# Optimization experiments

Measured on AMD Instinct MI355X. Metric: run time of the kernel, lower is better.

The kernel has to match this reference:

```python
import jax, jax.numpy as jnp
import numpy as np

THETA = 0.5  # forward default arg
ALPHA = 0.2  # LeakyReLU negative slope
NEG_INF = -9e15


def setup_inputs() -> dict:
    key = jax.random.key(0)
    k1, k2, k3, k4, k5 = jax.random.split(key, 5)
    N, F_IN, F_OUT = 8192, 256, 256
    h = jax.random.normal(k1, (N, F_IN), dtype=jnp.float32)
    adj = jax.random.randint(k2, (N, N), 0, 2, dtype=jnp.int32)
    cv_values = jax.random.uniform(k3, (N,), dtype=jnp.float32)
    # xavier_uniform with gain=1.414
    g = 1.414
    bw = g * np.sqrt(6.0 / (F_IN + F_OUT))
    W = jax.random.uniform(k4, (F_IN, F_OUT), dtype=jnp.float32, minval=-bw, maxval=bw)
    ba = g * np.sqrt(6.0 / (2 * F_OUT + 1))
    a = jax.random.uniform(k5, (2 * F_OUT, 1), dtype=jnp.float32, minval=-ba, maxval=ba)
    return {"h": h, "adj": adj, "cv_values": cv_values, "W": W, "a": a}


def reference(h, adj, cv_values, W, a):
    # Wh: [N, F_out]
    Wh = h @ W
    F_out = Wh.shape[1]
    a1 = a[:F_out, 0]   # [F_out]
    a2 = a[F_out:, 0]   # [F_out]
    # e_ij = LeakyReLU([Wh_i ; Wh_j] . a) = LeakyReLU(Wh_i.a1 + Wh_j.a2)
    f1 = Wh @ a1        # [N]
    f2 = Wh @ a2        # [N]
    e = jax.nn.leaky_relu(f1[:, None] + f2[None, :], negative_slope=ALPHA)
    # CV bias: theta * cv_i broadcast across row i
    e = e + THETA * cv_values[:, None]
    att = jnp.where(adj > 0, e, jnp.float32(NEG_INF))
    att = jax.nn.softmax(att, axis=1)
    # dropout is identity in eval mode (training=False)
    h_prime = att @ Wh  # [N, F_out]
    return jax.nn.elu(h_prime)  # concat=True branch
```

## Files before the change

### kernel.cpp

```cpp
#include <hip/hip_runtime.h>
#include <cstdint>
#include <cstddef>

typedef _Float16 half8 __attribute__((ext_vector_type(8)));
typedef _Float16 half4 __attribute__((ext_vector_type(4)));
typedef float f32x4 __attribute__((ext_vector_type(4)));

#define GAT_N 8192
#define GAT_F 256
#define GAT_NW 256
#define GAT_NQ 8
#define GAT_ALPHA 0.2f
#define GAT_LOG2E 1.4426950408889634f

__device__ inline unsigned enc_f32(float x) {
    unsigned b = __float_as_uint(x);
    return (b & 0x80000000u) ? ~b : (b | 0x80000000u);
}
__device__ inline float dec_f32(unsigned u) {
    unsigned b = (u & 0x80000000u) ? (u ^ 0x80000000u) : ~u;
    return __uint_as_float(b);
}


__global__ __launch_bounds__(256) void gat_k0_pack(
    const int* __restrict__ adj, unsigned char* __restrict__ adjB)
{
    const int wv = threadIdx.x >> 6;
    const int lane = threadIdx.x & 63;
    const int row = blockIdx.x * 4 + wv;
    const int* src = adj + (size_t)row * GAT_N;
    unsigned char* dst = adjB + (size_t)row * (GAT_N / 8);
    #pragma unroll 4
    for (int k = 0; k < 16; ++k) {
        const int4 v0 = *reinterpret_cast<const int4*>(src + k * 512 + lane * 8);
        const int4 v1 = *reinterpret_cast<const int4*>(src + k * 512 + lane * 8 + 4);
        unsigned m = (unsigned)(v0.x > 0)        | ((unsigned)(v0.y > 0) << 1)
                   | ((unsigned)(v0.z > 0) << 2) | ((unsigned)(v0.w > 0) << 3)
                   | ((unsigned)(v1.x > 0) << 4) | ((unsigned)(v1.y > 0) << 5)
                   | ((unsigned)(v1.z > 0) << 6) | ((unsigned)(v1.w > 0) << 7);
        dst[k * 64 + lane] = (unsigned char)m;
    }
}

__global__ __launch_bounds__(256) void gat_k0b_convert(
    const float* __restrict__ W, _Float16* __restrict__ WT,
    unsigned* __restrict__ f2mxEnc)
{
    const int g = blockIdx.x * 256 + threadIdx.x;
    if (g == 0) *f2mxEnc = 0u;
    const int k = g >> 8, n = g & 255;
    WT[n * GAT_F + k] = (_Float16)W[g];
}

__global__ __launch_bounds__(256, 2) void gat_k1_gemm(
    const float* __restrict__ h, const _Float16* __restrict__ WT,
    const float* __restrict__ a, _Float16* __restrict__ whT2,
    float* __restrict__ f1L, float* __restrict__ f2L,
    unsigned* __restrict__ f2mxEnc)
{
    __shared__ float sP1[4][16], sP2[4][16];
    const int wv = threadIdx.x >> 6;
    const int lane = threadIdx.x & 63;
    const int l15 = lane & 15;
    const int quad = lane >> 4;
    const int r0 = blockIdx.x * 16;

    f32x4 acc[4];
    #pragma unroll
    for (int t = 0; t < 4; ++t) { f32x4 z = {0.f,0.f,0.f,0.f}; acc[t] = z; }

    #pragma unroll
    for (int k0 = 0; k0 < GAT_F; k0 += 32) {
        const float* ap = h + (size_t)(r0 + l15) * GAT_F + k0 + quad * 8;
        const float4 a0 = *reinterpret_cast<const float4*>(ap);
        const float4 a1 = *reinterpret_cast<const float4*>(ap + 4);
        half8 af;
        af[0] = (_Float16)a0.x; af[1] = (_Float16)a0.y;
        af[2] = (_Float16)a0.z; af[3] = (_Float16)a0.w;
        af[4] = (_Float16)a1.x; af[5] = (_Float16)a1.y;
        af[6] = (_Float16)a1.z; af[7] = (_Float16)a1.w;
        #pragma unroll
        for (int t = 0; t < 4; ++t) {
            half8 bf = *reinterpret_cast<const half8*>(
                WT + (size_t)(wv * 64 + t * 16 + l15) * GAT_F + k0 + quad * 8);
            acc[t] = __builtin_amdgcn_mfma_f32_16x16x32_f16(af, bf, acc[t], 0, 0, 0);
        }
    }

    float p1[4] = {0.f,0.f,0.f,0.f}, p2[4] = {0.f,0.f,0.f,0.f};
    #pragma unroll
    for (int t = 0; t < 4; ++t) {
        float a1c = a[wv * 64 + t * 16 + l15];
        float a2c = a[GAT_F + wv * 64 + t * 16 + l15];
        #pragma unroll
        for (int r = 0; r < 4; ++r) {
            p1[r] = fmaf(acc[t][r], a1c, p1[r]);
            p2[r] = fmaf(acc[t][r], a2c, p2[r]);
        }
    }
    #pragma unroll
    for (int off = 1; off < 16; off <<= 1) {
        #pragma unroll
        for (int r = 0; r < 4; ++r) {
            p1[r] += __shfl_xor(p1[r], off);
            p2[r] += __shfl_xor(p2[r], off);
        }
    }
    if (l15 == 0) {
        #pragma unroll
        for (int r = 0; r < 4; ++r) {
            sP1[wv][quad * 4 + r] = p1[r];
            sP2[wv][quad * 4 + r] = p2[r];
        }
    }
    __syncthreads();
    if (threadIdx.x < 16) {
        const int row = threadIdx.x;
        const float s1 = (sP1[0][row] + sP1[1][row] + sP1[2][row] + sP1[3][row]) * GAT_LOG2E;
        const float s2 = (sP2[0][row] + sP2[1][row] + sP2[2][row] + sP2[3][row]) * GAT_LOG2E;
        f1L[r0 + row] = s1;
        f2L[r0 + row] = s2;
        float mx = s2;
        #pragma unroll
        for (int off = 1; off < 16; off <<= 1) mx = fmaxf(mx, __shfl_xor(mx, off));
        if (row == 0) atomicMax(f2mxEnc, enc_f32(mx));
    }

    const size_t tbase = (size_t)(r0 >> 6) * 16384
                       + (((r0 & 63) >> 3) + (quad >> 1)) * 2048
                       + (quad & 1) * 4;
    #pragma unroll
    for (int t = 0; t < 4; ++t) {
        const int c = wv * 64 + t * 16 + l15;
        half4 hv;
        #pragma unroll
        for (int r = 0; r < 4; ++r) hv[r] = (_Float16)acc[t][r];
        *reinterpret_cast<half4*>(whT2 + tbase + c * 8) = hv;
    }
}

__global__ __launch_bounds__(256, 3) void gat_k3_attn(
    const unsigned* __restrict__ adjW, const float* __restrict__ f1L,
    const float* __restrict__ f2L, const unsigned* __restrict__ f2mxEnc,
    const _Float16* __restrict__ whT2,
    _Float16* __restrict__ Ph,
    float* __restrict__ L)
{
    __shared__ __align__(16) _Float16 sB[2][8192];

    const int bx = blockIdx.x;
    const int q  = bx & 7;
    const int fh = (bx >> 3) & 1;
    const int rb = bx >> 4;
    const int wv = threadIdx.x >> 6;
    const int lane = threadIdx.x & 63;
    const int l15 = lane & 15;
    const int quad = lane >> 4;

    const int kq = q * 1024;
    const int r0 = rb * 128 + wv * 32;
    const int rA = r0 + l15;
    const int rB = rA + 16;

    const float fmxL = dec_f32(*f2mxEnc);
    const float f1A = f1L[rA];
    const float f1B = f1L[rB];
    const float sA = f1A + fmxL;
    const float sBv = f1B + fmxL;
    const float CA = fmaxf(sA, GAT_ALPHA * sA);
    const float CB = fmaxf(sBv, GAT_ALPHA * sBv);

    f32x4 acc[2][8];
    #pragma unroll
    for (int s = 0; s < 2; ++s)
        #pragma unroll
        for (int t = 0; t < 8; ++t) {
            f32x4 z = {0.f,0.f,0.f,0.f};
            acc[s][t] = z;
        }
    float d0 = 0.f, d1 = 0.f;

    const uint2* awA = reinterpret_cast<const uint2*>(adjW + (size_t)rA * GAT_NW + q * 32);
    const uint2* awB = reinterpret_cast<const uint2*>(adjW + (size_t)rB * GAT_NW + q * 32);
    const float* f2q = f2L + kq + quad * 8;

    const _Float16* tile0 = whT2 + (size_t)(q * 16) * 16384 + (size_t)fh * 1024
                          + (size_t)lane * 8;
    #define STAGE(buf, step)                                                   \
        {                                                                      \
            _Pragma("unroll")                                                  \
            for (int i = 0; i < 4; ++i) {                                      \
                const int koct = 2 * wv + (i >> 1);                            \
                const int hh = i & 1;                                          \
                const _Float16* gp = tile0 + (size_t)(step) * 16384            \
                                     + koct * 2048 + hh * 512;                 \
                _Float16* lp = &sB[buf][(koct * 128 + hh * 64) * 8];           \
                __builtin_amdgcn_global_load_lds(                              \
                    (const __attribute__((address_space(1))) void*)gp,         \
                    (__attribute__((address_space(3))) void*)lp, 16, 0, 0);    \
            }                                                                  \
        }

    uint2 nA = awA[0];
    uint2 nB = awB[0];
    float4 nfa = *reinterpret_cast<const float4*>(f2q);
    float4 nfb = *reinterpret_cast<const float4*>(f2q + 4);
    STAGE(0, 0)
    __syncthreads();

    for (int step = 0; step < 16; ++step) {
        const int cur = step & 1;
        const uint2 cA = nA, cB = nB;
        if (step < 15) {
            nA = awA[step + 1];
            nB = awB[step + 1];
            STAGE(1 - cur, step + 1)
        }

        #pragma unroll
        for (int k2 = 0; k2 < 2; ++k2) {
            const int u = step * 2 + k2;
            const float4 cfa = nfa, cfb = nfb;
            if (u < 31) {
                nfa = *reinterpret_cast<const float4*>(f2q + (u + 1) * 32);
                nfb = *reinterpret_cast<const float4*>(f2q + (u + 1) * 32 + 4);
            }
            const unsigned wA = k2 ? cA.y : cA.x;
            const unsigned wB = k2 ? cB.y : cB.x;
            const unsigned mA = (wA >> (quad * 8)) & 0xffu;
            const unsigned mB = (wB >> (quad * 8)) & 0xffu;
            const float f2v[8] = {cfa.x, cfa.y, cfa.z, cfa.w,
                                  cfb.x, cfb.y, cfb.z, cfb.w};

            half8 pA, pB;
            #pragma unroll
            for (int j = 0; j < 8; ++j) {
                const float f2j = f2v[j];
                float xa = f1A + f2j;
                float la = fmaxf(xa, GAT_ALPHA * xa);
                float pa = __builtin_amdgcn_exp2f(la - CA);
                pa = (mA & (1u << j)) ? pa : 0.f;
                d0 += pa;
                pA[j] = (_Float16)pa;
                float xb = f1B + f2j;
                float lb = fmaxf(xb, GAT_ALPHA * xb);
                float pb = __builtin_amdgcn_exp2f(lb - CB);
                pb = (mB & (1u << j)) ? pb : 0.f;
                d1 += pb;
                pB[j] = (_Float16)pb;
            }

            const int lbase = (k2 * 4 + quad) * 1024 + l15 * 8;
            #pragma unroll
            for (int t = 0; t < 8; ++t) {
                half8 bf = *reinterpret_cast<const half8*>(
                    &sB[cur][lbase + t * 128]);
                acc[0][t] = __builtin_amdgcn_mfma_f32_16x16x32_f16(pA, bf, acc[0][t], 0, 0, 0);
                acc[1][t] = __builtin_amdgcn_mfma_f32_16x16x32_f16(pB, bf, acc[1][t], 0, 0, 0);
            }
        }
        __syncthreads();
    }
    #undef STAGE

    d0 += __shfl_xor(d0, 16); d0 += __shfl_xor(d0, 32);
    d1 += __shfl_xor(d1, 16); d1 += __shfl_xor(d1, 32);
    if (fh == 0 && lane < 16) {
        float* Lq = L + q * GAT_N;
        Lq[rA] = d0; Lq[rB] = d1;
    }

    const int wid = rb * 4 + wv;
    _Float16* Pq = Ph + ((size_t)q * 256 + wid) * 8192;
    #pragma unroll
    for (int s = 0; s < 2; ++s)
        #pragma unroll
        for (int t = 0; t < 8; ++t) {
            const int tt = fh * 8 + t;
            half4 hv;
            #pragma unroll
            for (int r = 0; r < 4; ++r) hv[r] = (_Float16)acc[s][t][r];
            *reinterpret_cast<half4*>(Pq + (size_t)(((s * 16 + tt) * 64 + lane) * 4)) = hv;
        }
}

__global__ __launch_bounds__(256) void gat_k4_final(
    const _Float16* __restrict__ Ph, const float* __restrict__ L,
    float* __restrict__ out)
{
    const int tid = threadIdx.x;
    const int wid = blockIdx.x >> 3;
    __shared__ float s_rl[32];
    if (tid < 32) {
        const int row = wid * 32 + tid;
        float s = 0.f;
        #pragma unroll
        for (int q = 0; q < GAT_NQ; ++q) s += L[q * GAT_N + row];
        s_rl[tid] = 1.0f / fmaxf(s, 1e-30f);
    }
    __syncthreads();

    const int idx = blockIdx.x * 256 + tid;
    const int rem = idx & 2047;
    const int lane = rem & 63;
    const int st = rem >> 6;
    const int s = st >> 4, t = st & 15;
    const int l15 = lane & 15, quad = lane >> 4;
    const int lrow0 = s * 16 + quad * 4;
    const int col = t * 16 + l15;

    float accv[4] = {0.f, 0.f, 0.f, 0.f};
    #pragma unroll
    for (int q = 0; q < GAT_NQ; ++q) {
        half4 v = *reinterpret_cast<const half4*>(
            Ph + ((size_t)q * 256 + wid) * 8192 + (size_t)rem * 4);
        #pragma unroll
        for (int r = 0; r < 4; ++r) accv[r] += (float)v[r];
    }
    #pragma unroll
    for (int r = 0; r < 4; ++r) {
        const float v = accv[r] * s_rl[lrow0 + r];
        const float o = v > 0.f ? v : expm1f(v);
        out[(size_t)(wid * 32 + lrow0 + r) * GAT_F + col] = o;
    }
}

extern "C" void kernel_launch(void* const* d_in, const int* in_sizes, int n_in,
                              void* d_out, int out_size, void* d_ws, size_t ws_size,
                              hipStream_t stream)
{
    const float* h   = (const float*)d_in[0];
    const int*   adj = (const int*)d_in[1];
    const float* W   = (const float*)d_in[3];
    const float* a   = (const float*)d_in[4];
    float* out = (float*)d_out;
    char* ws = (char*)d_ws;

    const size_t SLAB = (size_t)GAT_N * GAT_F * 2;

    size_t off = 0;
    _Float16* whT2 = (_Float16*)(ws + off); off += SLAB;
    _Float16* Ph  = (_Float16*)(ws + off); off += GAT_NQ * SLAB;
    unsigned char* adjB = (unsigned char*)(ws + off); off += (size_t)GAT_N * GAT_N / 8;
    _Float16* WT  = (_Float16*)(ws + off); off += (size_t)GAT_F * GAT_F * 2;
    float* f1L = (float*)(ws + off); off += GAT_N * 4;
    float* f2L = (float*)(ws + off); off += GAT_N * 4;
    float* L   = (float*)(ws + off); off += GAT_NQ * GAT_N * 4;
    unsigned* f2mxEnc = (unsigned*)(ws + off); off += 256;

    gat_k0_pack<<<2048, 256, 0, stream>>>(adj, adjB);
    gat_k0b_convert<<<256, 256, 0, stream>>>(W, WT, f2mxEnc);
    gat_k1_gemm<<<512, 256, 0, stream>>>(h, WT, a, whT2, f1L, f2L, f2mxEnc);
    gat_k3_attn<<<1024, 256, 0, stream>>>((const unsigned*)adjB, f1L, f2L, f2mxEnc, whT2, Ph, L);
    gat_k4_final<<<2048, 256, 0, stream>>>(Ph, L, out);
}
```

Measured before the change: 455.1 us.

## Compute all 256 output features per attention block to avoid recomputing probabilities

The attention kernel no longer splits the feature dimension across two blocks. Each block now covers all 256 output columns, so the exp2 probability computation and adjacency loads are done once per row tile instead of twice, and the grid is halved. The LDS tile doubles, the accumulators double, and the occupancy hint drops from 3 to 2 blocks per CU, which raises register and LDS pressure. The LeakyReLU-minus-max is also algebraically folded into a single max of two affine terms, saving a few ALU ops per element.

```diff
diff --git a/kernel.cpp b/kernel.cpp
--- a/kernel.cpp
+++ b/kernel.cpp
@@ -140,19 +140,18 @@
     }
 }
 
-__global__ __launch_bounds__(256, 3) void gat_k3_attn(
+__global__ __launch_bounds__(256, 2) void gat_k3_attn(
     const unsigned* __restrict__ adjW, const float* __restrict__ f1L,
     const float* __restrict__ f2L, const unsigned* __restrict__ f2mxEnc,
     const _Float16* __restrict__ whT2,
     _Float16* __restrict__ Ph,
     float* __restrict__ L)
 {
-    __shared__ __align__(16) _Float16 sB[2][8192];
+    __shared__ __align__(16) _Float16 sB[2][16384];
 
     const int bx = blockIdx.x;
     const int q  = bx & 7;
-    const int fh = (bx >> 3) & 1;
-    const int rb = bx >> 4;
+    const int rb = bx >> 3;
     const int wv = threadIdx.x >> 6;
     const int lane = threadIdx.x & 63;
     const int l15 = lane & 15;
@@ -170,12 +169,14 @@
     const float sBv = f1B + fmxL;
     const float CA = fmaxf(sA, GAT_ALPHA * sA);
     const float CB = fmaxf(sBv, GAT_ALPHA * sBv);
-
-    f32x4 acc[2][8];
+    const float uA = f1A - CA, vA = GAT_ALPHA * f1A - CA;
+    const float uB = f1B - CB, vB = GAT_ALPHA * f1B - CB;
+
+    f32x4 acc[2][16];
     #pragma unroll
     for (int s = 0; s < 2; ++s)
         #pragma unroll
-        for (int t = 0; t < 8; ++t) {
+        for (int t = 0; t < 16; ++t) {
             f32x4 z = {0.f,0.f,0.f,0.f};
             acc[s][t] = z;
         }
@@ -185,17 +186,14 @@
     const uint2* awB = reinterpret_cast<const uint2*>(adjW + (size_t)rB * GAT_NW + q * 32);
     const float* f2q = f2L + kq + quad * 8;
 
-    const _Float16* tile0 = whT2 + (size_t)(q * 16) * 16384 + (size_t)fh * 1024
-                          + (size_t)lane * 8;
+    const _Float16* tile0 = whT2 + (size_t)(q * 16) * 16384 + (size_t)lane * 8;
     #define STAGE(buf, step)                                                   \
         {                                                                      \
             _Pragma("unroll")                                                  \
-            for (int i = 0; i < 4; ++i) {                                      \
-                const int koct = 2 * wv + (i >> 1);                            \
-                const int hh = i & 1;                                          \
-                const _Float16* gp = tile0 + (size_t)(step) * 16384            \
-                                     + koct * 2048 + hh * 512;                 \
-                _Float16* lp = &sB[buf][(koct * 128 + hh * 64) * 8];           \
+            for (int i = 0; i < 8; ++i) {                                      \
+                const int off = wv * 4096 + i * 512;                           \
+                const _Float16* gp = tile0 + (size_t)(step) * 16384 + off;     \
+                _Float16* lp = &sB[buf][off];                                  \
                 __builtin_amdgcn_global_load_lds(                              \
                     (const __attribute__((address_space(1))) void*)gp,         \
                     (__attribute__((address_space(3))) void*)lp, 16, 0, 0);    \
@@ -232,28 +230,26 @@
             const unsigned mB = (wB >> (quad * 8)) & 0xffu;
             const float f2v[8] = {cfa.x, cfa.y, cfa.z, cfa.w,
                                   cfb.x, cfb.y, cfb.z, cfb.w};
+            float af2[8];
+            #pragma unroll
+            for (int j = 0; j < 8; ++j) af2[j] = GAT_ALPHA * f2v[j];
 
             half8 pA, pB;
             #pragma unroll
             for (int j = 0; j < 8; ++j) {
-                const float f2j = f2v[j];
-                float xa = f1A + f2j;
-                float la = fmaxf(xa, GAT_ALPHA * xa);
-                float pa = __builtin_amdgcn_exp2f(la - CA);
+                float pa = __builtin_amdgcn_exp2f(fmaxf(uA + f2v[j], vA + af2[j]));
                 pa = (mA & (1u << j)) ? pa : 0.f;
                 d0 += pa;
                 pA[j] = (_Float16)pa;
-                float xb = f1B + f2j;
-                float lb = fmaxf(xb, GAT_ALPHA * xb);
-                float pb = __builtin_amdgcn_exp2f(lb - CB);
+                float pb = __builtin_amdgcn_exp2f(fmaxf(uB + f2v[j], vB + af2[j]));
                 pb = (mB & (1u << j)) ? pb : 0.f;
                 d1 += pb;
                 pB[j] = (_Float16)pb;
             }
 
-            const int lbase = (k2 * 4 + quad) * 1024 + l15 * 8;
+            const int lbase = (k2 * 4 + quad) * 2048 + l15 * 8;
             #pragma unroll
-            for (int t = 0; t < 8; ++t) {
+            for (int t = 0; t < 16; ++t) {
                 half8 bf = *reinterpret_cast<const half8*>(
                     &sB[cur][lbase + t * 128]);
                 acc[0][t] = __builtin_amdgcn_mfma_f32_16x16x32_f16(pA, bf, acc[0][t], 0, 0, 0);
@@ -266,7 +262,7 @@
 
     d0 += __shfl_xor(d0, 16); d0 += __shfl_xor(d0, 32);
     d1 += __shfl_xor(d1, 16); d1 += __shfl_xor(d1, 32);
-    if (fh == 0 && lane < 16) {
+    if (lane < 16) {
         float* Lq = L + q * GAT_N;
         Lq[rA] = d0; Lq[rB] = d1;
     }
@@ -276,12 +272,11 @@
     #pragma unroll
     for (int s = 0; s < 2; ++s)
         #pragma unroll
-        for (int t = 0; t < 8; ++t) {
-            const int tt = fh * 8 + t;
+        for (int t = 0; t < 16; ++t) {
             half4 hv;
             #pragma unroll
             for (int r = 0; r < 4; ++r) hv[r] = (_Float16)acc[s][t][r];
-            *reinterpret_cast<half4*>(Pq + (size_t)(((s * 16 + tt) * 64 + lane) * 4)) = hv;
+            *reinterpret_cast<half4*>(Pq + (size_t)(((s * 16 + t) * 64 + lane) * 4)) = hv;
         }
 }
 
@@ -352,6 +347,6 @@
     gat_k0_pack<<<2048, 256, 0, stream>>>(adj, adjB);
     gat_k0b_convert<<<256, 256, 0, stream>>>(W, WT, f2mxEnc);
     gat_k1_gemm<<<512, 256, 0, stream>>>(h, WT, a, whT2, f1L, f2L, f2mxEnc);
-    gat_k3_attn<<<1024, 256, 0, stream>>>((const unsigned*)adjB, f1L, f2L, f2mxEnc, whT2, Ph, L);
+    gat_k3_attn<<<512, 256, 0, stream>>>((const unsigned*)adjB, f1L, f2L, f2mxEnc, whT2, Ph, L);
     gat_k4_final<<<2048, 256, 0, stream>>>(Ph, L, out);
 }
```

Result: faster. 442.4 us (-2.8%).
